# Kernel optimization log

Measured on AMD Instinct MI355X. Metric: run time of the kernel, lower is better.

## Reference

```python
import jax, jax.numpy as jnp
import numpy as np

LENGTH = 128
BATCH = 256
MARGIN = 1.0
BONUS = 1000.0  # constraint bump applied to chart cells
NCELLS = LENGTH * (LENGTH + 1) // 2
NCONSTR = 8


def _offsets(length):
    off = np.zeros(length, dtype=np.int64)
    for lvl in range(1, length):
        off[lvl] = off[lvl - 1] + (length - (lvl - 1))
    return off

OFF = _offsets(LENGTH)


def _level_child_indices(length):
    # For each level: flat chart indices of left/right children, shape (L, N)
    idx = {}
    for level in range(1, length):
        L = length - level
        pos = np.arange(L)[:, None]
        n = np.arange(level)[None, :]
        l_idx = OFF[n] + pos                      # left child span (pos, width n)
        r_idx = OFF[level - 1 - n] + pos + n + 1  # right child span
        idx[level] = (jnp.asarray(l_idx), jnp.asarray(r_idx))
    return idx

IDX = _level_child_indices(LENGTH)


def _score_offsets(length):
    soff, acc = {}, 0
    for level in range(1, length):
        soff[level] = acc
        acc += (length - level) * level
    return soff, acc

SOFF, TOTAL = _score_offsets(LENGTH)


def setup_inputs():
    key = jax.random.key(0)
    k1, k2 = jax.random.split(key)
    scores = jax.random.normal(k1, (BATCH, TOTAL), dtype=jnp.float32)
    # constrained spans at level >= 1 (original skips level <= 0)
    constraint_pos = jax.random.randint(k2, (BATCH, NCONSTR), LENGTH, NCELLS, dtype=jnp.int32)
    return {"scores": scores, "constraint_pos": constraint_pos}


def _cky(scores, chart):
    # max-plus semiring inside DP, level by level over the triangular chart
    B = chart.shape[0]
    for level in range(1, LENGTH):
        L = LENGTH - level
        N = level
        l_idx, r_idx = IDX[level]
        ls = chart[:, l_idx]                                     # (B, L, N)
        rs = chart[:, r_idx]                                     # (B, L, N)
        xs = scores[:, SOFF[level]:SOFF[level] + L * N].reshape(B, L, N)
        best = jnp.max(ls + rs + xs, axis=2)                     # (B, L)
        off = int(OFF[level])
        chart = chart.at[:, off:off + L].add(best)
    return chart[:, -1]                                          # (B,) root scores


def reference(scores, constraint_pos):
    B = scores.shape[0]
    zero_chart = jnp.zeros((B, NCELLS), dtype=scores.dtype)
    rows = jnp.arange(B)[:, None]
    constr_chart = zero_chart.at[rows, constraint_pos].set(BONUS)
    subtract = jnp.full((B,), BONUS * constraint_pos.shape[1], dtype=scores.dtype)
    constr_s = _cky(scores, constr_chart) - subtract
    pred_s = _cky(scores, zero_chart)
    mask = (jnp.abs(pred_s - constr_s) >= 0.001).astype(scores.dtype)
    hinge = jnp.maximum(MARGIN + pred_s - constr_s, 0.0) * mask
    msum = mask.sum()
    return jnp.where(msum > 0.1, hinge.sum() / jnp.maximum(msum, 1.0), hinge.sum())
```

## Files before the change

### kernel.cpp

```cpp
#include <hip/hip_runtime.h>
#include <hip/hip_bf16.h>
#include <math.h>

#define LEN 128
#define NCELLS 8256
#define TOTAL 349504
#define NCONSTR 8
#define BONUS 1000.0f
#define NT 512

__device__ __forceinline__ void level_barrier() {
    __builtin_amdgcn_sched_barrier(0);
    asm volatile("s_waitcnt lgkmcnt(0)\n\ts_barrier" ::: "memory");
    __builtin_amdgcn_sched_barrier(0);
}

__device__ __forceinline__ float dpp_xor1_max(float v) {
    int r = __builtin_amdgcn_update_dpp(0, __float_as_int(v), 0xB1, 0xF, 0xF, true);
    return fmaxf(v, __int_as_float(r));
}
__device__ __forceinline__ float dpp_xor2_max(float v) {
    int r = __builtin_amdgcn_update_dpp(0, __float_as_int(v), 0x4E, 0xF, 0xF, true);
    return fmaxf(v, __int_as_float(r));
}

template<int LG>
__device__ __forceinline__ void redmax2(float& a, float& b) {
    #pragma unroll
    for (int mm = (1 << LG) >> 1; mm >= 4; mm >>= 1) {
        a = fmaxf(a, __shfl_xor(a, mm));
        b = fmaxf(b, __shfl_xor(b, mm));
    }
    if constexpr (LG >= 2) { a = dpp_xor2_max(a); b = dpp_xor2_max(b); }
    if constexpr (LG >= 1) { a = dpp_xor1_max(a); b = dpp_xor1_max(b); }
}

template<int LG, int LG2, int JM, int JM2>
__device__ __forceinline__ void lstep(const int level, int& soff,
        const float* __restrict__ g, float2* __restrict__ chart,
        float (&rcur)[16], float (&rnxt)[16], const int tid)
{
    const int N = level;
    const int L = LEN - level;
    constexpr int T = 1 << LG;
    const int pos = tid >> LG;
    const int sub = tid & (T - 1);
    const int soff_n = soff + L * N;

    if constexpr (LG2 >= 0) {
        constexpr int T2 = 1 << LG2;
        const int N2 = level + 1;
        const int L2 = L - 1;
        const int pos2 = tid >> LG2;
        const int sub2 = tid & (T2 - 1);
        if (pos2 < L2) {
            const float* __restrict__ gp = g + soff_n + pos2 * N2 + sub2;
            #pragma unroll
            for (int j = 0; j < JM2; j++) {
                if (sub2 + j * T2 < N2) rnxt[j] = gp[j * T2];
            }
        }
    }

    float bp = -INFINITY, bc = -INFINITY;
    if (pos < L) {
        const int jml = (N - sub + T - 1) >> LG;
        float2 lv[JM], rv[JM];
        float  xs[JM];
        #pragma unroll
        for (int j = 0; j < JM; j++) {
            const int n = sub + j * T;
            const int m = level - 1 - n;
            const bool v = (j < jml);
            const int l_idx = ((n * (257 - n)) >> 1) + pos;
            int r_idx = ((m * (257 - m)) >> 1) + pos + n + 1;
            r_idx = v ? r_idx : 0;
            lv[j] = chart[l_idx];
            rv[j] = chart[r_idx];
            xs[j] = v ? rcur[j] : -INFINITY;
        }
        #pragma unroll
        for (int j = 0; j < JM; j++) {
            bp = fmaxf(bp, lv[j].x + rv[j].x + xs[j]);
            bc = fmaxf(bc, lv[j].y + rv[j].y + xs[j]);
        }
    }
    redmax2<LG>(bp, bc);
    if (pos < L && sub == 0) {
        const int q = ((level * (257 - level)) >> 1) + pos;
        float2 c = chart[q];
        c.x += bp;
        c.y += bc;
        chart[q] = c;
    }
    level_barrier();
    soff = soff_n;
}

template<int K>
__device__ __forceinline__ void seg4(int& soff, const float* __restrict__ g,
        float2* __restrict__ chart, float (&rA)[16], float (&rB)[16], const int tid)
{
    const int l0 = 4 * K - 3;
    #pragma unroll 1
    for (int l = l0; l < l0 + 4; l += 2) {
        lstep<2, 2, K, K + 1>(l,     soff, g, chart, rA, rB, tid);
        lstep<2, 2, K, K + 1>(l + 1, soff, g, chart, rB, rA, tid);
    }
}

__global__ __launch_bounds__(NT)
void cky_fused_kernel(const float* __restrict__ scores,
                      const int* __restrict__ cpos,
                      float* __restrict__ ws)
{
    __shared__ float2 chart[NCELLS];

    const int b   = blockIdx.x;
    const int tid = threadIdx.x;
    const float* __restrict__ g = scores + (size_t)b * TOTAL;

    float rA[16], rB[16];

    {
        const int pos = tid >> 2;
        const int sub = tid & 3;
        if (pos < 127 && sub == 0) rA[0] = g[pos];
    }
    int cp = -1;
    if (tid < NCONSTR) cp = cpos[b * NCONSTR + tid];

    for (int i = tid; i < NCELLS; i += NT) chart[i] = make_float2(0.f, 0.f);
    level_barrier();
    if (tid < NCONSTR) chart[cp].y = BONUS;
    level_barrier();

    int soff = 0;

    seg4<1>(soff, g, chart, rA, rB, tid);
    seg4<2>(soff, g, chart, rA, rB, tid);
    seg4<3>(soff, g, chart, rA, rB, tid);
    seg4<4>(soff, g, chart, rA, rB, tid);
    seg4<5>(soff, g, chart, rA, rB, tid);
    seg4<6>(soff, g, chart, rA, rB, tid);
    seg4<7>(soff, g, chart, rA, rB, tid);
    seg4<8>(soff, g, chart, rA, rB, tid);
    seg4<9>(soff, g, chart, rA, rB, tid);
    seg4<10>(soff, g, chart, rA, rB, tid);
    seg4<11>(soff, g, chart, rA, rB, tid);
    seg4<12>(soff, g, chart, rA, rB, tid);
    seg4<13>(soff, g, chart, rA, rB, tid);
    seg4<14>(soff, g, chart, rA, rB, tid);
    seg4<15>(soff, g, chart, rA, rB, tid);
    lstep<2,2,16,16>(61, soff, g, chart, rA, rB, tid);
    lstep<2,2,16,16>(62, soff, g, chart, rB, rA, tid);
    lstep<2,3,16,8>(63, soff, g, chart, rA, rB, tid);
    lstep<3,3,8,9>(64, soff, g, chart, rB, rA, tid);
    #pragma unroll 1
    for (int l = 65; l < 72; l += 2) {
        lstep<3,3,9,10>(l,     soff, g, chart, rA, rB, tid);
        lstep<3,3,9,10>(l + 1, soff, g, chart, rB, rA, tid);
    }
    #pragma unroll 1
    for (int l = 73; l < 80; l += 2) {
        lstep<3,3,10,11>(l,     soff, g, chart, rA, rB, tid);
        lstep<3,3,10,11>(l + 1, soff, g, chart, rB, rA, tid);
    }
    #pragma unroll 1
    for (int l = 81; l < 88; l += 2) {
        lstep<3,3,11,12>(l,     soff, g, chart, rA, rB, tid);
        lstep<3,3,11,12>(l + 1, soff, g, chart, rB, rA, tid);
    }
    #pragma unroll 1
    for (int l = 89; l < 94; l += 2) {
        lstep<3,3,12,12>(l,     soff, g, chart, rA, rB, tid);
        lstep<3,3,12,12>(l + 1, soff, g, chart, rB, rA, tid);
    }
    lstep<3,4,12,6>(95, soff, g, chart, rA, rB, tid);
    lstep<4,4,6,7>(96, soff, g, chart, rB, rA, tid);
    #pragma unroll 1
    for (int l = 97; l < 110; l += 2) {
        lstep<4,4,7,7>(l,     soff, g, chart, rA, rB, tid);
        lstep<4,4,7,7>(l + 1, soff, g, chart, rB, rA, tid);
    }
    lstep<4,5,7,4>(111, soff, g, chart, rA, rB, tid);
    lstep<5,5,4,4>(112, soff, g, chart, rB, rA, tid);
    #pragma unroll 1
    for (int l = 113; l < 118; l += 2) {
        lstep<5,5,4,4>(l,     soff, g, chart, rA, rB, tid);
        lstep<5,5,4,4>(l + 1, soff, g, chart, rB, rA, tid);
    }
    lstep<5,6,4,2>(119, soff, g, chart, rA, rB, tid);
    lstep<6,6,2,2>(120, soff, g, chart, rB, rA, tid);
    #pragma unroll 1
    for (int l = 121; l < 126; l += 2) {
        lstep<6,6,2,2>(l,     soff, g, chart, rA, rB, tid);
        lstep<6,6,2,2>(l + 1, soff, g, chart, rB, rA, tid);
    }
    lstep<6,-1,2,2>(127, soff, g, chart, rA, rB, tid);

    if (tid == 0) {
        const float2 f = chart[NCELLS - 1];
        const float pred   = f.x;
        const float constr = f.y - BONUS * NCONSTR;
        const float diff   = pred - constr;
        const float mask   = (fabsf(diff) >= 0.001f) ? 1.f : 0.f;
        const float hinge  = fmaxf(1.0f + diff, 0.f) * mask;
        atomicAdd(ws + 0, hinge);
        atomicAdd(ws + 1, mask);
    }
}

__global__ void final_kernel(const float* __restrict__ ws, float* __restrict__ out) {
    const float h = ws[0];
    const float m = ws[1];
    out[0] = (m > 0.1f) ? (h / fmaxf(m, 1.f)) : h;
}

extern "C" void kernel_launch(void* const* d_in, const int* in_sizes, int n_in,
                              void* d_out, int out_size, void* d_ws, size_t ws_size,
                              hipStream_t stream) {
    const float* scores = (const float*)d_in[0];
    const int*   cpos   = (const int*)d_in[1];
    float* out = (float*)d_out;
    float* ws  = (float*)d_ws;

    hipMemsetAsync(ws, 0, 2 * sizeof(float), stream);
    cky_fused_kernel<<<dim3(256), dim3(NT), 0, stream>>>(scores, cpos, ws);
    final_kernel<<<dim3(1), dim3(1), 0, stream>>>(ws, out);
}
```

Before: 142.1 us.

## Prefetch scores two levels ahead and finish last levels in one wavefront

The score register prefetch now runs two levels ahead using a triple-rotated register set (rA/rB/rC), so each global load has more time to land before use. The scores for the final 16 levels are staged into shared memory at kernel start. Those levels then run on a single 64-lane wavefront, which needs no block-wide barriers. This is meant to cut global-load latency stalls and the barrier overhead of the narrow tail levels. In exchange it uses more registers and more LDS, which may lower occupancy, and it fully unrolls the level schedule.

```diff
diff --git a/kernel.cpp b/kernel.cpp
--- a/kernel.cpp
+++ b/kernel.cpp
@@ -8,6 +8,9 @@
 #define NCONSTR 8
 #define BONUS 1000.0f
 #define NT 512
+#define TB_TOTAL 15912
+#define TB_SOFF 333592
+#define TB_VEC 3978
 
 __device__ __forceinline__ void level_barrier() {
     __builtin_amdgcn_sched_barrier(0);
@@ -49,12 +52,13 @@
 
     if constexpr (LG2 >= 0) {
         constexpr int T2 = 1 << LG2;
-        const int N2 = level + 1;
-        const int L2 = L - 1;
+        const int N2 = level + 2;
+        const int L2 = L - 2;
+        const int soff_nn = soff_n + (L - 1) * (N + 1);
         const int pos2 = tid >> LG2;
         const int sub2 = tid & (T2 - 1);
         if (pos2 < L2) {
-            const float* __restrict__ gp = g + soff_n + pos2 * N2 + sub2;
+            const float* __restrict__ gp = g + soff_nn + pos2 * N2 + sub2;
             #pragma unroll
             for (int j = 0; j < JM2; j++) {
                 if (sub2 + j * T2 < N2) rnxt[j] = gp[j * T2];
@@ -99,14 +103,52 @@
 
 template<int K>
 __device__ __forceinline__ void seg4(int& soff, const float* __restrict__ g,
-        float2* __restrict__ chart, float (&rA)[16], float (&rB)[16], const int tid)
+        float2* __restrict__ chart, float (&X)[16], float (&Y)[16], float (&Z)[16],
+        const int tid)
 {
-    const int l0 = 4 * K - 3;
-    #pragma unroll 1
-    for (int l = l0; l < l0 + 4; l += 2) {
-        lstep<2, 2, K, K + 1>(l,     soff, g, chart, rA, rB, tid);
-        lstep<2, 2, K, K + 1>(l + 1, soff, g, chart, rB, rA, tid);
-    }
+    lstep<2,2,K,K>  (4*K-3, soff, g, chart, X, Z, tid);
+    lstep<2,2,K,K>  (4*K-2, soff, g, chart, Y, X, tid);
+    lstep<2,2,K,K+1>(4*K-1, soff, g, chart, Z, Y, tid);
+    lstep<2,2,K,K+1>(4*K,   soff, g, chart, X, Z, tid);
+}
+
+template<int LGT>
+__device__ __forceinline__ void tail_level(const int level, int& tb,
+        float2* __restrict__ chart, const float* __restrict__ sc, const int lane)
+{
+    const int N = level, L = LEN - level;
+    constexpr int T = 1 << LGT;
+    const int pos = lane >> LGT;
+    const int sub = lane & (T - 1);
+    const bool act = (pos < L);
+    const int jmax = (N + T - 1) >> LGT;
+    const int base = tb + pos * N;
+    float bp = -INFINITY, bc = -INFINITY;
+    #pragma unroll 4
+    for (int j = 0; j < jmax; j++) {
+        const int n = sub + j * T;
+        const bool v = act && (n < N);
+        const int m = level - 1 - n;
+        int l_idx = ((n * (257 - n)) >> 1) + pos;
+        int r_idx = ((m * (257 - m)) >> 1) + pos + n + 1;
+        l_idx = v ? l_idx : 0;
+        r_idx = v ? r_idx : 0;
+        const float2 lv = chart[l_idx];
+        const float2 rv = chart[r_idx];
+        const float x = v ? sc[base + (n < N ? n : 0)] : -INFINITY;
+        bp = fmaxf(bp, lv.x + rv.x + x);
+        bc = fmaxf(bc, lv.y + rv.y + x);
+    }
+    redmax2<LGT>(bp, bc);
+    if (act && sub == 0) {
+        const int q = ((level * (257 - level)) >> 1) + pos;
+        float2 c = chart[q];
+        c.x += bp;
+        c.y += bc;
+        chart[q] = c;
+    }
+    asm volatile("s_waitcnt lgkmcnt(0)" ::: "memory");
+    tb += L * N;
 }
 
 __global__ __launch_bounds__(NT)
@@ -115,89 +157,124 @@
                       float* __restrict__ ws)
 {
     __shared__ float2 chart[NCELLS];
+    __shared__ float4 sc4[TB_VEC];
 
     const int b   = blockIdx.x;
     const int tid = threadIdx.x;
     const float* __restrict__ g = scores + (size_t)b * TOTAL;
 
-    float rA[16], rB[16];
-
+    float rA[16], rB[16], rC[16];
+
+    float4 tt[8];
+    {
+        const float4* __restrict__ g4 = (const float4*)(g + TB_SOFF);
+        #pragma unroll
+        for (int k = 0; k < 8; k++) {
+            const int i4 = tid + (k << 9);
+            if (i4 < TB_VEC) tt[k] = g4[i4];
+        }
+    }
     {
         const int pos = tid >> 2;
         const int sub = tid & 3;
         if (pos < 127 && sub == 0) rA[0] = g[pos];
-    }
-    int cp = -1;
+        if (pos < 126 && sub < 2)  rB[0] = g[127 + pos * 2 + sub];
+    }
+    int cp = 0;
     if (tid < NCONSTR) cp = cpos[b * NCONSTR + tid];
 
     for (int i = tid; i < NCELLS; i += NT) chart[i] = make_float2(0.f, 0.f);
+    #pragma unroll
+    for (int k = 0; k < 8; k++) {
+        const int i4 = tid + (k << 9);
+        if (i4 < TB_VEC) sc4[i4] = tt[k];
+    }
     level_barrier();
     if (tid < NCONSTR) chart[cp].y = BONUS;
     level_barrier();
 
     int soff = 0;
 
-    seg4<1>(soff, g, chart, rA, rB, tid);
-    seg4<2>(soff, g, chart, rA, rB, tid);
-    seg4<3>(soff, g, chart, rA, rB, tid);
-    seg4<4>(soff, g, chart, rA, rB, tid);
-    seg4<5>(soff, g, chart, rA, rB, tid);
-    seg4<6>(soff, g, chart, rA, rB, tid);
-    seg4<7>(soff, g, chart, rA, rB, tid);
-    seg4<8>(soff, g, chart, rA, rB, tid);
-    seg4<9>(soff, g, chart, rA, rB, tid);
-    seg4<10>(soff, g, chart, rA, rB, tid);
-    seg4<11>(soff, g, chart, rA, rB, tid);
-    seg4<12>(soff, g, chart, rA, rB, tid);
-    seg4<13>(soff, g, chart, rA, rB, tid);
-    seg4<14>(soff, g, chart, rA, rB, tid);
-    seg4<15>(soff, g, chart, rA, rB, tid);
-    lstep<2,2,16,16>(61, soff, g, chart, rA, rB, tid);
-    lstep<2,2,16,16>(62, soff, g, chart, rB, rA, tid);
-    lstep<2,3,16,8>(63, soff, g, chart, rA, rB, tid);
-    lstep<3,3,8,9>(64, soff, g, chart, rB, rA, tid);
-    #pragma unroll 1
-    for (int l = 65; l < 72; l += 2) {
-        lstep<3,3,9,10>(l,     soff, g, chart, rA, rB, tid);
-        lstep<3,3,9,10>(l + 1, soff, g, chart, rB, rA, tid);
-    }
-    #pragma unroll 1
-    for (int l = 73; l < 80; l += 2) {
-        lstep<3,3,10,11>(l,     soff, g, chart, rA, rB, tid);
-        lstep<3,3,10,11>(l + 1, soff, g, chart, rB, rA, tid);
-    }
-    #pragma unroll 1
-    for (int l = 81; l < 88; l += 2) {
-        lstep<3,3,11,12>(l,     soff, g, chart, rA, rB, tid);
-        lstep<3,3,11,12>(l + 1, soff, g, chart, rB, rA, tid);
-    }
-    #pragma unroll 1
-    for (int l = 89; l < 94; l += 2) {
-        lstep<3,3,12,12>(l,     soff, g, chart, rA, rB, tid);
-        lstep<3,3,12,12>(l + 1, soff, g, chart, rB, rA, tid);
-    }
-    lstep<3,4,12,6>(95, soff, g, chart, rA, rB, tid);
-    lstep<4,4,6,7>(96, soff, g, chart, rB, rA, tid);
-    #pragma unroll 1
-    for (int l = 97; l < 110; l += 2) {
-        lstep<4,4,7,7>(l,     soff, g, chart, rA, rB, tid);
-        lstep<4,4,7,7>(l + 1, soff, g, chart, rB, rA, tid);
-    }
-    lstep<4,5,7,4>(111, soff, g, chart, rA, rB, tid);
-    lstep<5,5,4,4>(112, soff, g, chart, rB, rA, tid);
-    #pragma unroll 1
-    for (int l = 113; l < 118; l += 2) {
-        lstep<5,5,4,4>(l,     soff, g, chart, rA, rB, tid);
-        lstep<5,5,4,4>(l + 1, soff, g, chart, rB, rA, tid);
-    }
-    lstep<5,6,4,2>(119, soff, g, chart, rA, rB, tid);
-    lstep<6,6,2,2>(120, soff, g, chart, rB, rA, tid);
-    #pragma unroll 1
-    for (int l = 121; l < 126; l += 2) {
-        lstep<6,6,2,2>(l,     soff, g, chart, rA, rB, tid);
-        lstep<6,6,2,2>(l + 1, soff, g, chart, rB, rA, tid);
-    }
-    lstep<6,-1,2,2>(127, soff, g, chart, rA, rB, tid);
+    seg4<1>(soff, g, chart, rA, rB, rC, tid);
+    seg4<2>(soff, g, chart, rB, rC, rA, tid);
+    seg4<3>(soff, g, chart, rC, rA, rB, tid);
+    seg4<4>(soff, g, chart, rA, rB, rC, tid);
+    seg4<5>(soff, g, chart, rB, rC, rA, tid);
+    seg4<6>(soff, g, chart, rC, rA, rB, tid);
+    seg4<7>(soff, g, chart, rA, rB, rC, tid);
+    seg4<8>(soff, g, chart, rB, rC, rA, tid);
+    seg4<9>(soff, g, chart, rC, rA, rB, tid);
+    seg4<10>(soff, g, chart, rA, rB, rC, tid);
+    seg4<11>(soff, g, chart, rB, rC, rA, tid);
+    seg4<12>(soff, g, chart, rC, rA, rB, tid);
+    seg4<13>(soff, g, chart, rA, rB, rC, tid);
+    seg4<14>(soff, g, chart, rB, rC, rA, tid);
+    seg4<15>(soff, g, chart, rC, rA, rB, tid);
+    lstep<2,2,16,16>(61, soff, g, chart, rA, rC, tid);
+    lstep<2,3,16,8> (62, soff, g, chart, rB, rA, tid);
+    lstep<2,3,16,9> (63, soff, g, chart, rC, rB, tid);
+    lstep<3,3,8,9>  (64, soff, g, chart, rA, rC, tid);
+    lstep<3,3,9,9>  (65, soff, g, chart, rB, rA, tid);
+    lstep<3,3,9,9>  (66, soff, g, chart, rC, rB, tid);
+    lstep<3,3,9,9>  (67, soff, g, chart, rA, rC, tid);
+    lstep<3,3,9,9>  (68, soff, g, chart, rB, rA, tid);
+    lstep<3,3,9,9>  (69, soff, g, chart, rC, rB, tid);
+    lstep<3,3,9,9>  (70, soff, g, chart, rA, rC, tid);
+    lstep<3,3,9,10> (71, soff, g, chart, rB, rA, tid);
+    lstep<3,3,9,10> (72, soff, g, chart, rC, rB, tid);
+    lstep<3,3,10,10>(73, soff, g, chart, rA, rC, tid);
+    lstep<3,3,10,10>(74, soff, g, chart, rB, rA, tid);
+    lstep<3,3,10,10>(75, soff, g, chart, rC, rB, tid);
+    lstep<3,3,10,10>(76, soff, g, chart, rA, rC, tid);
+    lstep<3,3,10,10>(77, soff, g, chart, rB, rA, tid);
+    lstep<3,3,10,10>(78, soff, g, chart, rC, rB, tid);
+    lstep<3,3,10,11>(79, soff, g, chart, rA, rC, tid);
+    lstep<3,3,10,11>(80, soff, g, chart, rB, rA, tid);
+    lstep<3,3,11,11>(81, soff, g, chart, rC, rB, tid);
+    lstep<3,3,11,11>(82, soff, g, chart, rA, rC, tid);
+    lstep<3,3,11,11>(83, soff, g, chart, rB, rA, tid);
+    lstep<3,3,11,11>(84, soff, g, chart, rC, rB, tid);
+    lstep<3,3,11,11>(85, soff, g, chart, rA, rC, tid);
+    lstep<3,3,11,11>(86, soff, g, chart, rB, rA, tid);
+    lstep<3,3,11,12>(87, soff, g, chart, rC, rB, tid);
+    lstep<3,3,11,12>(88, soff, g, chart, rA, rC, tid);
+    lstep<3,3,12,12>(89, soff, g, chart, rB, rA, tid);
+    lstep<3,3,12,12>(90, soff, g, chart, rC, rB, tid);
+    lstep<3,3,12,12>(91, soff, g, chart, rA, rC, tid);
+    lstep<3,3,12,12>(92, soff, g, chart, rB, rA, tid);
+    lstep<3,3,12,12>(93, soff, g, chart, rC, rB, tid);
+    lstep<3,4,12,6> (94, soff, g, chart, rA, rC, tid);
+    lstep<3,4,12,7> (95, soff, g, chart, rB, rA, tid);
+    lstep<4,4,6,7>  (96, soff, g, chart, rC, rB, tid);
+    lstep<4,4,7,7>  (97, soff, g, chart, rA, rC, tid);
+    lstep<4,4,7,7>  (98, soff, g, chart, rB, rA, tid);
+    lstep<4,4,7,7>  (99, soff, g, chart, rC, rB, tid);
+    lstep<4,4,7,7> (100, soff, g, chart, rA, rC, tid);
+    lstep<4,4,7,7> (101, soff, g, chart, rB, rA, tid);
+    lstep<4,4,7,7> (102, soff, g, chart, rC, rB, tid);
+    lstep<4,4,7,7> (103, soff, g, chart, rA, rC, tid);
+    lstep<4,4,7,7> (104, soff, g, chart, rB, rA, tid);
+    lstep<4,4,7,7> (105, soff, g, chart, rC, rB, tid);
+    lstep<4,4,7,7> (106, soff, g, chart, rA, rC, tid);
+    lstep<4,4,7,7> (107, soff, g, chart, rB, rA, tid);
+    lstep<4,4,7,7> (108, soff, g, chart, rC, rB, tid);
+    lstep<4,4,7,7> (109, soff, g, chart, rA, rC, tid);
+    lstep<4,-1,7,0>(110, soff, g, chart, rB, rA, tid);
+    lstep<4,-1,7,0>(111, soff, g, chart, rC, rB, tid);
+
+    if (tid >= 64) return;
+    {
+        const float* __restrict__ sc = (const float*)sc4;
+        int tb = 0;
+        #pragma unroll 1
+        for (int l = 112; l < 120; ++l) tail_level<2>(l, tb, chart, sc, tid);
+        #pragma unroll 1
+        for (int l = 120; l < 124; ++l) tail_level<3>(l, tb, chart, sc, tid);
+        tail_level<4>(124, tb, chart, sc, tid);
+        tail_level<4>(125, tb, chart, sc, tid);
+        tail_level<5>(126, tb, chart, sc, tid);
+        tail_level<6>(127, tb, chart, sc, tid);
+    }
 
     if (tid == 0) {
         const float2 f = chart[NCELLS - 1];
```

New measurement: 169.8 us. +19.5%, slower.

## Split pred and constrained CKY charts into separate blocks, reduce in final kernel

Applied to the files above, without the earlier changes.

Each block previously ran both charts (prediction and constrained) as float2 pairs in one shared chart. Now the grid doubles to 512 blocks, and each block runs one chart of plain floats, chosen by blockIdx. Per-batch root scores go to workspace, and a 256-thread final kernel computes the hinge and mask with a wave-shuffle reduction, which removes the memset and atomics. This gives more blocks to fill the 256 compute units and halves per-block shared memory and reduction work, at the cost of loading each batch's scores twice.

```diff
diff --git a/kernel.cpp b/kernel.cpp
--- a/kernel.cpp
+++ b/kernel.cpp
@@ -25,19 +25,17 @@
 }
 
 template<int LG>
-__device__ __forceinline__ void redmax2(float& a, float& b) {
+__device__ __forceinline__ void redmax(float& a) {
     #pragma unroll
-    for (int mm = (1 << LG) >> 1; mm >= 4; mm >>= 1) {
+    for (int mm = (1 << LG) >> 1; mm >= 4; mm >>= 1)
         a = fmaxf(a, __shfl_xor(a, mm));
-        b = fmaxf(b, __shfl_xor(b, mm));
-    }
-    if constexpr (LG >= 2) { a = dpp_xor2_max(a); b = dpp_xor2_max(b); }
-    if constexpr (LG >= 1) { a = dpp_xor1_max(a); b = dpp_xor1_max(b); }
+    if constexpr (LG >= 2) a = dpp_xor2_max(a);
+    if constexpr (LG >= 1) a = dpp_xor1_max(a);
 }
 
 template<int LG, int LG2, int JM, int JM2>
 __device__ __forceinline__ void lstep(const int level, int& soff,
-        const float* __restrict__ g, float2* __restrict__ chart,
+        const float* __restrict__ g, float* __restrict__ chart,
         float (&rcur)[16], float (&rnxt)[16], const int tid)
 {
     const int N = level;
@@ -62,11 +60,10 @@
         }
     }
 
-    float bp = -INFINITY, bc = -INFINITY;
+    float bp = -INFINITY;
     if (pos < L) {
         const int jml = (N - sub + T - 1) >> LG;
-        float2 lv[JM], rv[JM];
-        float  xs[JM];
+        float lv[JM], rv[JM], xs[JM];
         #pragma unroll
         for (int j = 0; j < JM; j++) {
             const int n = sub + j * T;
@@ -80,26 +77,19 @@
             xs[j] = v ? rcur[j] : -INFINITY;
         }
         #pragma unroll
-        for (int j = 0; j < JM; j++) {
-            bp = fmaxf(bp, lv[j].x + rv[j].x + xs[j]);
-            bc = fmaxf(bc, lv[j].y + rv[j].y + xs[j]);
-        }
-    }
-    redmax2<LG>(bp, bc);
-    if (pos < L && sub == 0) {
-        const int q = ((level * (257 - level)) >> 1) + pos;
-        float2 c = chart[q];
-        c.x += bp;
-        c.y += bc;
-        chart[q] = c;
-    }
+        for (int j = 0; j < JM; j++)
+            bp = fmaxf(bp, lv[j] + rv[j] + xs[j]);
+    }
+    redmax<LG>(bp);
+    if (pos < L && sub == 0)
+        chart[((level * (257 - level)) >> 1) + pos] += bp;
     level_barrier();
     soff = soff_n;
 }
 
 template<int K>
 __device__ __forceinline__ void seg4(int& soff, const float* __restrict__ g,
-        float2* __restrict__ chart, float (&rA)[16], float (&rB)[16], const int tid)
+        float* __restrict__ chart, float (&rA)[16], float (&rB)[16], const int tid)
 {
     const int l0 = 4 * K - 3;
     #pragma unroll 1
@@ -110,14 +100,16 @@
 }
 
 __global__ __launch_bounds__(NT)
-void cky_fused_kernel(const float* __restrict__ scores,
-                      const int* __restrict__ cpos,
-                      float* __restrict__ ws)
+void cky_kernel(const float* __restrict__ scores,
+                const int* __restrict__ cpos,
+                float* __restrict__ roots)
 {
-    __shared__ float2 chart[NCELLS];
-
-    const int b   = blockIdx.x;
-    const int tid = threadIdx.x;
+    __shared__ float chart[NCELLS];
+
+    const int bb   = blockIdx.x;
+    const int b    = bb & 255;
+    const int kind = bb >> 8;
+    const int tid  = threadIdx.x;
     const float* __restrict__ g = scores + (size_t)b * TOTAL;
 
     float rA[16], rB[16];
@@ -127,12 +119,12 @@
         const int sub = tid & 3;
         if (pos < 127 && sub == 0) rA[0] = g[pos];
     }
-    int cp = -1;
+    int cp = 0;
     if (tid < NCONSTR) cp = cpos[b * NCONSTR + tid];
 
-    for (int i = tid; i < NCELLS; i += NT) chart[i] = make_float2(0.f, 0.f);
+    for (int i = tid; i < NCELLS; i += NT) chart[i] = 0.f;
     level_barrier();
-    if (tid < NCONSTR) chart[cp].y = BONUS;
+    if (kind && tid < NCONSTR) chart[cp] = BONUS;
     level_barrier();
 
     int soff = 0;
@@ -154,8 +146,8 @@
     seg4<15>(soff, g, chart, rA, rB, tid);
     lstep<2,2,16,16>(61, soff, g, chart, rA, rB, tid);
     lstep<2,2,16,16>(62, soff, g, chart, rB, rA, tid);
-    lstep<2,3,16,8>(63, soff, g, chart, rA, rB, tid);
-    lstep<3,3,8,9>(64, soff, g, chart, rB, rA, tid);
+    lstep<2,3,16,8> (63, soff, g, chart, rA, rB, tid);
+    lstep<3,3,8,9>  (64, soff, g, chart, rB, rA, tid);
     #pragma unroll 1
     for (int l = 65; l < 72; l += 2) {
         lstep<3,3,9,10>(l,     soff, g, chart, rA, rB, tid);
@@ -176,8 +168,8 @@
         lstep<3,3,12,12>(l,     soff, g, chart, rA, rB, tid);
         lstep<3,3,12,12>(l + 1, soff, g, chart, rB, rA, tid);
     }
-    lstep<3,4,12,6>(95, soff, g, chart, rA, rB, tid);
-    lstep<4,4,6,7>(96, soff, g, chart, rB, rA, tid);
+    lstep<3,4,12,6> (95, soff, g, chart, rA, rB, tid);
+    lstep<4,4,6,7>  (96, soff, g, chart, rB, rA, tid);
     #pragma unroll 1
     for (int l = 97; l < 110; l += 2) {
         lstep<4,4,7,7>(l,     soff, g, chart, rA, rB, tid);
@@ -199,22 +191,32 @@
     }
     lstep<6,-1,2,2>(127, soff, g, chart, rA, rB, tid);
 
-    if (tid == 0) {
-        const float2 f = chart[NCELLS - 1];
-        const float pred   = f.x;
-        const float constr = f.y - BONUS * NCONSTR;
-        const float diff   = pred - constr;
-        const float mask   = (fabsf(diff) >= 0.001f) ? 1.f : 0.f;
-        const float hinge  = fmaxf(1.0f + diff, 0.f) * mask;
-        atomicAdd(ws + 0, hinge);
-        atomicAdd(ws + 1, mask);
-    }
-}
-
-__global__ void final_kernel(const float* __restrict__ ws, float* __restrict__ out) {
-    const float h = ws[0];
-    const float m = ws[1];
-    out[0] = (m > 0.1f) ? (h / fmaxf(m, 1.f)) : h;
+    if (tid == 0) roots[bb] = chart[NCELLS - 1];
+}
+
+__global__ __launch_bounds__(256)
+void final_kernel(const float* __restrict__ roots, float* __restrict__ out) {
+    const int t = threadIdx.x;
+    const float pred   = roots[t];
+    const float constr = roots[256 + t] - BONUS * NCONSTR;
+    const float diff   = pred - constr;
+    const float mask   = (fabsf(diff) >= 0.001f) ? 1.f : 0.f;
+    float h = fmaxf(1.0f + diff, 0.f) * mask;
+    float m = mask;
+    #pragma unroll
+    for (int s = 32; s > 0; s >>= 1) {
+        h += __shfl_xor(h, s);
+        m += __shfl_xor(m, s);
+    }
+    __shared__ float sh[8];
+    const int w = t >> 6;
+    if ((t & 63) == 0) { sh[w] = h; sh[4 + w] = m; }
+    __syncthreads();
+    if (t == 0) {
+        const float H = sh[0] + sh[1] + sh[2] + sh[3];
+        const float M = sh[4] + sh[5] + sh[6] + sh[7];
+        out[0] = (M > 0.1f) ? (H / fmaxf(M, 1.f)) : H;
+    }
 }
 
 extern "C" void kernel_launch(void* const* d_in, const int* in_sizes, int n_in,
@@ -222,10 +224,9 @@
                               hipStream_t stream) {
     const float* scores = (const float*)d_in[0];
     const int*   cpos   = (const int*)d_in[1];
-    float* out = (float*)d_out;
-    float* ws  = (float*)d_ws;
-
-    hipMemsetAsync(ws, 0, 2 * sizeof(float), stream);
-    cky_fused_kernel<<<dim3(256), dim3(NT), 0, stream>>>(scores, cpos, ws);
-    final_kernel<<<dim3(1), dim3(1), 0, stream>>>(ws, out);
-}
+    float* out   = (float*)d_out;
+    float* roots = (float*)d_ws;
+
+    cky_kernel<<<dim3(512), dim3(NT), 0, stream>>>(scores, cpos, roots);
+    final_kernel<<<dim3(1), dim3(256), 0, stream>>>(roots, out);
+}
```

Measured after the change: 257.1 us. 81.0% more time.

## Prefetch next level's chart operands before barrier and fold constraint bonus into writes

Applied to the files above, without the earlier changes.

Before each level's barrier, every thread issues the LDS loads for the next level's child cells whose inputs are already final. It waits only partially on lgkmcnt, so those reads overlap the barrier and the reduction. The one dependency produced by the current level is loaded after the barrier. The constraint bonus is applied by comparing against register-held positions at write time, so the chart no longer needs a read-modify-write, level 1 is handled specially, and launch bounds request 2 blocks per CU. This raises register pressure and adds index-selection logic.

```diff
diff --git a/kernel.cpp b/kernel.cpp
--- a/kernel.cpp
+++ b/kernel.cpp
@@ -3,15 +3,38 @@
 #include <math.h>
 
 #define LEN 128
-#define NCELLS 8256
+#define NCELLS_PAD 8384
 #define TOTAL 349504
 #define NCONSTR 8
 #define BONUS 1000.0f
 #define NT 512
-
-__device__ __forceinline__ void level_barrier() {
+#define PMAX 7
+
+__device__ __forceinline__ int OFFi(int n) { return (n * (257 - n)) >> 1; }
+
+template<int N> __device__ __forceinline__ void wait_lgkm() {
+    static_assert(N >= 0 && N <= 15, "lgkmcnt range");
+    if constexpr (N == 0)  asm volatile("s_waitcnt lgkmcnt(0)" ::: "memory");
+    else if constexpr (N == 1)  asm volatile("s_waitcnt lgkmcnt(1)" ::: "memory");
+    else if constexpr (N == 2)  asm volatile("s_waitcnt lgkmcnt(2)" ::: "memory");
+    else if constexpr (N == 3)  asm volatile("s_waitcnt lgkmcnt(3)" ::: "memory");
+    else if constexpr (N == 4)  asm volatile("s_waitcnt lgkmcnt(4)" ::: "memory");
+    else if constexpr (N == 5)  asm volatile("s_waitcnt lgkmcnt(5)" ::: "memory");
+    else if constexpr (N == 6)  asm volatile("s_waitcnt lgkmcnt(6)" ::: "memory");
+    else if constexpr (N == 7)  asm volatile("s_waitcnt lgkmcnt(7)" ::: "memory");
+    else if constexpr (N == 8)  asm volatile("s_waitcnt lgkmcnt(8)" ::: "memory");
+    else if constexpr (N == 9)  asm volatile("s_waitcnt lgkmcnt(9)" ::: "memory");
+    else if constexpr (N == 10) asm volatile("s_waitcnt lgkmcnt(10)" ::: "memory");
+    else if constexpr (N == 11) asm volatile("s_waitcnt lgkmcnt(11)" ::: "memory");
+    else if constexpr (N == 12) asm volatile("s_waitcnt lgkmcnt(12)" ::: "memory");
+    else if constexpr (N == 13) asm volatile("s_waitcnt lgkmcnt(13)" ::: "memory");
+    else if constexpr (N == 14) asm volatile("s_waitcnt lgkmcnt(14)" ::: "memory");
+    else                        asm volatile("s_waitcnt lgkmcnt(15)" ::: "memory");
+}
+
+__device__ __forceinline__ void bar() {
     __builtin_amdgcn_sched_barrier(0);
-    asm volatile("s_waitcnt lgkmcnt(0)\n\ts_barrier" ::: "memory");
+    asm volatile("s_barrier" ::: "memory");
     __builtin_amdgcn_sched_barrier(0);
 }
 
@@ -23,7 +46,6 @@
     int r = __builtin_amdgcn_update_dpp(0, __float_as_int(v), 0x4E, 0xF, 0xF, true);
     return fmaxf(v, __int_as_float(r));
 }
-
 template<int LG>
 __device__ __forceinline__ void redmax2(float& a, float& b) {
     #pragma unroll
@@ -35,17 +57,47 @@
     if constexpr (LG >= 1) { a = dpp_xor1_max(a); b = dpp_xor1_max(b); }
 }
 
+__device__ __forceinline__ bool chit(int q, const int4& c0, const int4& c1) {
+    return (q == c0.x) | (q == c0.y) | (q == c0.z) | (q == c0.w) |
+           (q == c1.x) | (q == c1.y) | (q == c1.z) | (q == c1.w);
+}
+
 template<int LG, int LG2, int JM, int JM2>
 __device__ __forceinline__ void lstep(const int level, int& soff,
         const float* __restrict__ g, float2* __restrict__ chart,
-        float (&rcur)[16], float (&rnxt)[16], const int tid)
+        float (&rcur)[16], float (&rnxt)[16],
+        float2 (&calv)[PMAX], float2 (&carv)[PMAX],
+        float2 (&cblv)[PMAX], float2 (&cbrv)[PMAX],
+        const int4 cc0, const int4 cc1, const int tid)
 {
     const int N = level;
     const int L = LEN - level;
     constexpr int T = 1 << LG;
+    constexpr int P = (JM < PMAX) ? JM : PMAX;
     const int pos = tid >> LG;
     const int sub = tid & (T - 1);
     const int soff_n = soff + L * N;
+
+    const int rowm1 = OFFi(N - 1);
+    const int pcap  = 127 - N;
+    const int pdep  = (pos < pcap) ? pos : pcap;
+    const float2 dlv = chart[rowm1 + pdep];
+    const float2 drv = chart[rowm1 + pdep + 1];
+
+    float2 plv[(JM > P) ? (JM - P) : 1];
+    float2 prv[(JM > P) ? (JM - P) : 1];
+    if constexpr (JM > P) {
+        #pragma unroll
+        for (int j = P; j < JM; j++) {
+            const int n = sub + j * T;
+            const int m = N - 1 - n;
+            const bool v = (n <= N - 1);
+            const int li = OFFi(n) + pos;
+            const int ri = v ? (OFFi(m) + pos + n + 1) : 0;
+            plv[j - P] = chart[li];
+            prv[j - P] = chart[ri];
+        }
+    }
 
     if constexpr (LG2 >= 0) {
         constexpr int T2 = 1 << LG2;
@@ -56,151 +108,214 @@
         if (pos2 < L2) {
             const float* __restrict__ gp = g + soff_n + pos2 * N2 + sub2;
             #pragma unroll
-            for (int j = 0; j < JM2; j++) {
+            for (int j = 0; j < JM2; j++)
                 if (sub2 + j * T2 < N2) rnxt[j] = gp[j * T2];
-            }
         }
     }
 
     float bp = -INFINITY, bc = -INFINITY;
     if (pos < L) {
-        const int jml = (N - sub + T - 1) >> LG;
-        float2 lv[JM], rv[JM];
-        float  xs[JM];
         #pragma unroll
-        for (int j = 0; j < JM; j++) {
+        for (int j = 0; j < P; j++) {
             const int n = sub + j * T;
-            const int m = level - 1 - n;
-            const bool v = (j < jml);
-            const int l_idx = ((n * (257 - n)) >> 1) + pos;
-            int r_idx = ((m * (257 - m)) >> 1) + pos + n + 1;
-            r_idx = v ? r_idx : 0;
-            lv[j] = chart[l_idx];
-            rv[j] = chart[r_idx];
-            xs[j] = v ? rcur[j] : -INFINITY;
-        }
+            float2 lv = calv[j];
+            if constexpr (JM <= PMAX) {
+                const bool isdep = (n == N - 1);
+                lv.x = isdep ? dlv.x : lv.x;
+                lv.y = isdep ? dlv.y : lv.y;
+            }
+            float2 rv = carv[j];
+            if (j == 0) {
+                const bool r0 = (sub == 0);
+                rv.x = r0 ? drv.x : rv.x;
+                rv.y = r0 ? drv.y : rv.y;
+            }
+            const float x = (n < N) ? rcur[j] : -INFINITY;
+            bp = fmaxf(bp, lv.x + rv.x + x);
+            bc = fmaxf(bc, lv.y + rv.y + x);
+        }
+        if constexpr (JM > P) {
+            #pragma unroll
+            for (int j = P; j < JM; j++) {
+                const int n = sub + j * T;
+                const float x = (n < N) ? rcur[j] : -INFINITY;
+                bp = fmaxf(bp, plv[j - P].x + prv[j - P].x + x);
+                bc = fmaxf(bc, plv[j - P].y + prv[j - P].y + x);
+            }
+        }
+    }
+    redmax2<LG>(bp, bc);
+
+    if (pos < L && sub == 0) {
+        const int q = OFFi(N) + pos;
+        chart[q] = make_float2(bp, bc + (chit(q, cc0, cc1) ? BONUS : 0.0f));
+    }
+
+    if constexpr (LG2 >= 0) {
+        constexpr int T2 = 1 << LG2;
+        constexpr int P2 = (JM2 < PMAX) ? JM2 : PMAX;
+        const int pos2 = tid >> LG2;
+        const int sub2 = tid & (T2 - 1);
         #pragma unroll
-        for (int j = 0; j < JM; j++) {
-            bp = fmaxf(bp, lv[j].x + rv[j].x + xs[j]);
-            bc = fmaxf(bc, lv[j].y + rv[j].y + xs[j]);
-        }
-    }
-    redmax2<LG>(bp, bc);
-    if (pos < L && sub == 0) {
-        const int q = ((level * (257 - level)) >> 1) + pos;
-        float2 c = chart[q];
-        c.x += bp;
-        c.y += bc;
-        chart[q] = c;
-    }
-    level_barrier();
+        for (int j = 0; j < P2; j++) {
+            const int n2 = sub2 + j * T2;
+            int li = OFFi(n2) + pos2;
+            int ri;
+            if constexpr (JM2 <= PMAX) {
+                li = (n2 == N) ? 0 : li;
+                const int m2 = N - n2;
+                ri = (n2 >= 1 && n2 <= N) ? (OFFi(m2) + pos2 + n2 + 1) : 0;
+            } else {
+                const int m2 = N - n2;
+                ri = (n2 >= 1) ? (OFFi(m2) + pos2 + n2 + 1) : 0;
+            }
+            cblv[j] = chart[li];
+            cbrv[j] = chart[ri];
+        }
+        wait_lgkm<(2 * P2 <= 14) ? 2 * P2 : 14>();
+        bar();
+    } else {
+        wait_lgkm<0>();
+        bar();
+    }
     soff = soff_n;
 }
 
 template<int K>
 __device__ __forceinline__ void seg4(int& soff, const float* __restrict__ g,
-        float2* __restrict__ chart, float (&rA)[16], float (&rB)[16], const int tid)
+        float2* __restrict__ chart, float (&rA)[16], float (&rB)[16],
+        float2 (&Ulv)[PMAX], float2 (&Urv)[PMAX], float2 (&Vlv)[PMAX], float2 (&Vrv)[PMAX],
+        const int4 cc0, const int4 cc1, const int tid)
 {
     const int l0 = 4 * K - 3;
     #pragma unroll 1
     for (int l = l0; l < l0 + 4; l += 2) {
-        lstep<2, 2, K, K + 1>(l,     soff, g, chart, rA, rB, tid);
-        lstep<2, 2, K, K + 1>(l + 1, soff, g, chart, rB, rA, tid);
-    }
-}
-
-__global__ __launch_bounds__(NT)
+        lstep<2,2,K,K+1>(l,   soff, g, chart, rA, rB, Vlv, Vrv, Ulv, Urv, cc0, cc1, tid);
+        lstep<2,2,K,K+1>(l+1, soff, g, chart, rB, rA, Ulv, Urv, Vlv, Vrv, cc0, cc1, tid);
+    }
+}
+
+__global__ __launch_bounds__(NT, 2)
 void cky_fused_kernel(const float* __restrict__ scores,
                       const int* __restrict__ cpos,
                       float* __restrict__ ws)
 {
-    __shared__ float2 chart[NCELLS];
+    __shared__ float2 chart[NCELLS_PAD];
 
     const int b   = blockIdx.x;
     const int tid = threadIdx.x;
     const float* __restrict__ g = scores + (size_t)b * TOTAL;
 
     float rA[16], rB[16];
+    float2 Ulv[PMAX], Urv[PMAX], Vlv[PMAX], Vrv[PMAX];
+
+    const int4 cc0 = ((const int4*)(cpos + b * NCONSTR))[0];
+    const int4 cc1 = ((const int4*)(cpos + b * NCONSTR))[1];
 
     {
-        const int pos = tid >> 2;
-        const int sub = tid & 3;
-        if (pos < 127 && sub == 0) rA[0] = g[pos];
-    }
-    int cp = -1;
-    if (tid < NCONSTR) cp = cpos[b * NCONSTR + tid];
-
-    for (int i = tid; i < NCELLS; i += NT) chart[i] = make_float2(0.f, 0.f);
-    level_barrier();
-    if (tid < NCONSTR) chart[cp].y = BONUS;
-    level_barrier();
-
-    int soff = 0;
-
-    seg4<1>(soff, g, chart, rA, rB, tid);
-    seg4<2>(soff, g, chart, rA, rB, tid);
-    seg4<3>(soff, g, chart, rA, rB, tid);
-    seg4<4>(soff, g, chart, rA, rB, tid);
-    seg4<5>(soff, g, chart, rA, rB, tid);
-    seg4<6>(soff, g, chart, rA, rB, tid);
-    seg4<7>(soff, g, chart, rA, rB, tid);
-    seg4<8>(soff, g, chart, rA, rB, tid);
-    seg4<9>(soff, g, chart, rA, rB, tid);
-    seg4<10>(soff, g, chart, rA, rB, tid);
-    seg4<11>(soff, g, chart, rA, rB, tid);
-    seg4<12>(soff, g, chart, rA, rB, tid);
-    seg4<13>(soff, g, chart, rA, rB, tid);
-    seg4<14>(soff, g, chart, rA, rB, tid);
-    seg4<15>(soff, g, chart, rA, rB, tid);
-    lstep<2,2,16,16>(61, soff, g, chart, rA, rB, tid);
-    lstep<2,2,16,16>(62, soff, g, chart, rB, rA, tid);
-    lstep<2,3,16,8>(63, soff, g, chart, rA, rB, tid);
-    lstep<3,3,8,9>(64, soff, g, chart, rB, rA, tid);
+        const int pos = tid >> 2, sub = tid & 3;
+        if (sub == 0 && pos < 127) rA[0] = g[pos];
+        if (sub < 2 && pos < 126)  rB[0] = g[127 + pos * 2 + sub];
+    }
+
+    #pragma unroll
+    for (int k = 0; k < 17; k++) {
+        const int i = tid + k * NT;
+        if (i < NCELLS_PAD) chart[i] = make_float2(0.f, 0.f);
+    }
+    wait_lgkm<0>();
+    bar();
+
+    {
+        const int pos = tid >> 2, sub = tid & 3;
+        const bool act = (sub == 0 && pos < 127);
+        float bp = act ? rA[0] : -INFINITY;
+        float bc = bp;
+        redmax2<2>(bp, bc);
+        if (act) {
+            const int q = OFFi(1) + pos;
+            chart[q] = make_float2(bp, bc + (chit(q, cc0, cc1) ? BONUS : 0.0f));
+        }
+        {
+            const int n2 = sub;
+            int li = OFFi(n2) + pos;
+            li = (n2 == 1) ? 0 : li;
+            const int ri = (n2 == 1) ? (OFFi(0) + pos + 2) : 0;
+            Ulv[0] = chart[li];
+            Urv[0] = chart[ri];
+        }
+        wait_lgkm<2>();
+        bar();
+    }
+
+    int soff = 127;
+
+    lstep<2,2,1,1>(2, soff, g, chart, rB, rA, Ulv, Urv, Vlv, Vrv, cc0, cc1, tid);
+    lstep<2,2,1,1>(3, soff, g, chart, rA, rB, Vlv, Vrv, Ulv, Urv, cc0, cc1, tid);
+    lstep<2,2,1,2>(4, soff, g, chart, rB, rA, Ulv, Urv, Vlv, Vrv, cc0, cc1, tid);
+    seg4<2>(soff, g, chart, rA, rB, Ulv, Urv, Vlv, Vrv, cc0, cc1, tid);
+    seg4<3>(soff, g, chart, rA, rB, Ulv, Urv, Vlv, Vrv, cc0, cc1, tid);
+    seg4<4>(soff, g, chart, rA, rB, Ulv, Urv, Vlv, Vrv, cc0, cc1, tid);
+    seg4<5>(soff, g, chart, rA, rB, Ulv, Urv, Vlv, Vrv, cc0, cc1, tid);
+    seg4<6>(soff, g, chart, rA, rB, Ulv, Urv, Vlv, Vrv, cc0, cc1, tid);
+    seg4<7>(soff, g, chart, rA, rB, Ulv, Urv, Vlv, Vrv, cc0, cc1, tid);
+    seg4<8>(soff, g, chart, rA, rB, Ulv, Urv, Vlv, Vrv, cc0, cc1, tid);
+    seg4<9>(soff, g, chart, rA, rB, Ulv, Urv, Vlv, Vrv, cc0, cc1, tid);
+    seg4<10>(soff, g, chart, rA, rB, Ulv, Urv, Vlv, Vrv, cc0, cc1, tid);
+    seg4<11>(soff, g, chart, rA, rB, Ulv, Urv, Vlv, Vrv, cc0, cc1, tid);
+    seg4<12>(soff, g, chart, rA, rB, Ulv, Urv, Vlv, Vrv, cc0, cc1, tid);
+    seg4<13>(soff, g, chart, rA, rB, Ulv, Urv, Vlv, Vrv, cc0, cc1, tid);
+    seg4<14>(soff, g, chart, rA, rB, Ulv, Urv, Vlv, Vrv, cc0, cc1, tid);
+    seg4<15>(soff, g, chart, rA, rB, Ulv, Urv, Vlv, Vrv, cc0, cc1, tid);
+    lstep<2,2,16,16>(61, soff, g, chart, rA, rB, Vlv, Vrv, Ulv, Urv, cc0, cc1, tid);
+    lstep<2,2,16,16>(62, soff, g, chart, rB, rA, Ulv, Urv, Vlv, Vrv, cc0, cc1, tid);
+    lstep<2,3,16,8> (63, soff, g, chart, rA, rB, Vlv, Vrv, Ulv, Urv, cc0, cc1, tid);
+    lstep<3,3,8,9>  (64, soff, g, chart, rB, rA, Ulv, Urv, Vlv, Vrv, cc0, cc1, tid);
     #pragma unroll 1
     for (int l = 65; l < 72; l += 2) {
-        lstep<3,3,9,10>(l,     soff, g, chart, rA, rB, tid);
-        lstep<3,3,9,10>(l + 1, soff, g, chart, rB, rA, tid);
+        lstep<3,3,9,10>(l,   soff, g, chart, rA, rB, Vlv, Vrv, Ulv, Urv, cc0, cc1, tid);
+        lstep<3,3,9,10>(l+1, soff, g, chart, rB, rA, Ulv, Urv, Vlv, Vrv, cc0, cc1, tid);
     }
     #pragma unroll 1
     for (int l = 73; l < 80; l += 2) {
-        lstep<3,3,10,11>(l,     soff, g, chart, rA, rB, tid);
-        lstep<3,3,10,11>(l + 1, soff, g, chart, rB, rA, tid);
+        lstep<3,3,10,11>(l,   soff, g, chart, rA, rB, Vlv, Vrv, Ulv, Urv, cc0, cc1, tid);
+        lstep<3,3,10,11>(l+1, soff, g, chart, rB, rA, Ulv, Urv, Vlv, Vrv, cc0, cc1, tid);
     }
     #pragma unroll 1
     for (int l = 81; l < 88; l += 2) {
-        lstep<3,3,11,12>(l,     soff, g, chart, rA, rB, tid);
-        lstep<3,3,11,12>(l + 1, soff, g, chart, rB, rA, tid);
+        lstep<3,3,11,12>(l,   soff, g, chart, rA, rB, Vlv, Vrv, Ulv, Urv, cc0, cc1, tid);
+        lstep<3,3,11,12>(l+1, soff, g, chart, rB, rA, Ulv, Urv, Vlv, Vrv, cc0, cc1, tid);
     }
     #pragma unroll 1
     for (int l = 89; l < 94; l += 2) {
-        lstep<3,3,12,12>(l,     soff, g, chart, rA, rB, tid);
-        lstep<3,3,12,12>(l + 1, soff, g, chart, rB, rA, tid);
-    }
-    lstep<3,4,12,6>(95, soff, g, chart, rA, rB, tid);
-    lstep<4,4,6,7>(96, soff, g, chart, rB, rA, tid);
+        lstep<3,3,12,12>(l,   soff, g, chart, rA, rB, Vlv, Vrv, Ulv, Urv, cc0, cc1, tid);
+        lstep<3,3,12,12>(l+1, soff, g, chart, rB, rA, Ulv, Urv, Vlv, Vrv, cc0, cc1, tid);
+    }
+    lstep<3,4,12,6> (95, soff, g, chart, rA, rB, Vlv, Vrv, Ulv, Urv, cc0, cc1, tid);
+    lstep<4,4,6,7>  (96, soff, g, chart, rB, rA, Ulv, Urv, Vlv, Vrv, cc0, cc1, tid);
     #pragma unroll 1
     for (int l = 97; l < 110; l += 2) {
-        lstep<4,4,7,7>(l,     soff, g, chart, rA, rB, tid);
-        lstep<4,4,7,7>(l + 1, soff, g, chart, rB, rA, tid);
-    }
-    lstep<4,5,7,4>(111, soff, g, chart, rA, rB, tid);
-    lstep<5,5,4,4>(112, soff, g, chart, rB, rA, tid);
+        lstep<4,4,7,7>(l,   soff, g, chart, rA, rB, Vlv, Vrv, Ulv, Urv, cc0, cc1, tid);
+        lstep<4,4,7,7>(l+1, soff, g, chart, rB, rA, Ulv, Urv, Vlv, Vrv, cc0, cc1, tid);
+    }
+    lstep<4,5,7,4>(111, soff, g, chart, rA, rB, Vlv, Vrv, Ulv, Urv, cc0, cc1, tid);
+    lstep<5,5,4,4>(112, soff, g, chart, rB, rA, Ulv, Urv, Vlv, Vrv, cc0, cc1, tid);
     #pragma unroll 1
     for (int l = 113; l < 118; l += 2) {
-        lstep<5,5,4,4>(l,     soff, g, chart, rA, rB, tid);
-        lstep<5,5,4,4>(l + 1, soff, g, chart, rB, rA, tid);
-    }
-    lstep<5,6,4,2>(119, soff, g, chart, rA, rB, tid);
-    lstep<6,6,2,2>(120, soff, g, chart, rB, rA, tid);
+        lstep<5,5,4,4>(l,   soff, g, chart, rA, rB, Vlv, Vrv, Ulv, Urv, cc0, cc1, tid);
+        lstep<5,5,4,4>(l+1, soff, g, chart, rB, rA, Ulv, Urv, Vlv, Vrv, cc0, cc1, tid);
+    }
+    lstep<5,6,4,2>(119, soff, g, chart, rA, rB, Vlv, Vrv, Ulv, Urv, cc0, cc1, tid);
+    lstep<6,6,2,2>(120, soff, g, chart, rB, rA, Ulv, Urv, Vlv, Vrv, cc0, cc1, tid);
     #pragma unroll 1
     for (int l = 121; l < 126; l += 2) {
-        lstep<6,6,2,2>(l,     soff, g, chart, rA, rB, tid);
-        lstep<6,6,2,2>(l + 1, soff, g, chart, rB, rA, tid);
-    }
-    lstep<6,-1,2,2>(127, soff, g, chart, rA, rB, tid);
+        lstep<6,6,2,2>(l,   soff, g, chart, rA, rB, Vlv, Vrv, Ulv, Urv, cc0, cc1, tid);
+        lstep<6,6,2,2>(l+1, soff, g, chart, rB, rA, Ulv, Urv, Vlv, Vrv, cc0, cc1, tid);
+    }
+    lstep<6,-1,2,0>(127, soff, g, chart, rA, rB, Vlv, Vrv, Ulv, Urv, cc0, cc1, tid);
 
     if (tid == 0) {
-        const float2 f = chart[NCELLS - 1];
+        const float2 f = chart[OFFi(127)];
         const float pred   = f.x;
         const float constr = f.y - BONUS * NCONSTR;
         const float diff   = pred - constr;
```

Measured after the change: 173.0 us. 21.7% more time.
